# Performance work log

Measured on AMD Instinct MI355X. Metric: run time of the kernel, lower is better.

Reference implementation:

```python
import jax, jax.numpy as jnp
import numpy as np

B, T, C = 2, 2048, 2048
H = 16
ROPE_DIM, NOPE_DIM, V_DIM = 64, 64, 128
HEAD_DIM = NOPE_DIM + ROPE_DIM  # 128
Q_RANK, KV_RANK = 1536, 512


def setup_inputs() -> dict:
    key = jax.random.key(0)
    ks = jax.random.split(key, 8)
    std = 0.02
    return {
        "x": jax.random.normal(ks[0], (B, T, C), jnp.float32),
        "cos": jax.random.normal(ks[1], (1, T, 1, ROPE_DIM // 2), jnp.float32),
        "sin": jax.random.normal(ks[2], (1, T, 1, ROPE_DIM // 2), jnp.float32),
        "wq_down": jax.random.normal(ks[3], (Q_RANK, C), jnp.float32) * std,
        "wq_up": jax.random.normal(ks[4], (H * HEAD_DIM, Q_RANK), jnp.float32) * std,
        "wkv_down": jax.random.normal(ks[5], (KV_RANK, C), jnp.float32) * std,
        "wkv_up": jax.random.normal(ks[6], (H * (HEAD_DIM + V_DIM), KV_RANK), jnp.float32) * std,
        "wo": jax.random.normal(ks[7], (C, H * V_DIM), jnp.float32) * std,
    }


def _rope(x, cos, sin):
    # x: [B, T, H, rope_dim]
    d = x.shape[-1] // 2
    x1, x2 = x[..., :d], x[..., d:]
    return jnp.concatenate([x1 * cos + x2 * sin, -x1 * sin + x2 * cos], axis=-1)


def _rms_norm(x):
    eps = jnp.finfo(x.dtype).eps
    return x * jax.lax.rsqrt(jnp.mean(jnp.square(x), axis=-1, keepdims=True) + eps)


def reference(x, cos, sin, wq_down, wq_up, wkv_down, wkv_up, wo):
    # Low-rank q projection
    q = jnp.einsum('btc,rc,dr->btd', x, wq_down, wq_up)
    q = q.reshape(B, T, H, HEAD_DIM)
    q_nope, q_rope = q[..., :NOPE_DIM], q[..., NOPE_DIM:]
    # Low-rank kv projection (naive decompression)
    kv = jnp.einsum('btc,rc,dr->btd', x, wkv_down, wkv_up)
    kv = kv.reshape(B, T, H, HEAD_DIM + V_DIM)
    k_nope = kv[..., :NOPE_DIM]
    k_rope = kv[..., NOPE_DIM:HEAD_DIM]
    v = kv[..., HEAD_DIM:]
    # Partial RoPE on the rope sub-dims only
    q_rope = _rope(q_rope, cos, sin)
    k_rope = _rope(k_rope, cos, sin)
    q = _rms_norm(jnp.concatenate([q_nope, q_rope], axis=-1))
    k = _rms_norm(jnp.concatenate([k_nope, k_rope], axis=-1))
    # Causal SDPA: [B, H, T, T]
    scale = 1.0 / jnp.sqrt(jnp.float32(HEAD_DIM))
    scores = jnp.einsum('bthd,bshd->bhts', q, k) * scale
    causal = jnp.tril(jnp.ones((T, T), dtype=bool))
    scores = jnp.where(causal, scores, jnp.finfo(scores.dtype).min)
    probs = jax.nn.softmax(scores, axis=-1)
    y = jnp.einsum('bhts,bshd->bthd', probs, v).reshape(B, T, H * V_DIM)
    return y @ wo.T
```

## Files before the change

kernel.cpp:

```cpp
#include <hip/hip_runtime.h>
#include <hip/hip_bf16.h>
#include <math.h>
#include <type_traits>

#define AS1 __attribute__((address_space(1)))
#define AS3 __attribute__((address_space(3)))

typedef __bf16  bf16x8 __attribute__((ext_vector_type(8)));
typedef float   f32x4  __attribute__((ext_vector_type(4)));
typedef __hip_bfloat16 bf16;

#define MFMA16x16x32 __builtin_amdgcn_mfma_f32_16x16x32_bf16

__device__ __forceinline__ void gload16(const void* g, void* l) {
  __builtin_amdgcn_global_load_lds((const AS1 void*)g, (AS3 void*)l, 16, 0, 0);
}

__device__ __forceinline__ unsigned short bfbits(float v) {
  return __builtin_bit_cast(unsigned short, __float2bfloat16(v));
}

struct CastArgs {
  const float4* src[6];
  ushort4* dst[6];
  unsigned bound[6];
};

__global__ __launch_bounds__(256) void f2bf_multi(CastArgs a) {
  unsigned i = blockIdx.x * 256 + threadIdx.x;
  if (i >= a.bound[5]) return;
  unsigned lo = 0;
  int s = 0;
#pragma unroll
  for (int k = 0; k < 5; k++) {
    if (i >= a.bound[k]) { s = k + 1; lo = a.bound[k]; }
  }
  unsigned idx = i - lo;
  float4 v = a.src[s][idx];
  ushort4 o;
  o.x = bfbits(v.x); o.y = bfbits(v.y); o.z = bfbits(v.z); o.w = bfbits(v.w);
  a.dst[s][idx] = o;
}

template <typename OutT>
__global__ __launch_bounds__(256, 3) void gemm_bt(const bf16* __restrict__ A,
                                                  const bf16* __restrict__ W,
                                                  OutT* __restrict__ Cp,
                                                  int M, int N, int K, int lda) {
  __shared__ __align__(16) bf16 As[128 * 32];
  __shared__ __align__(16) bf16 Ws[128 * 32];
  const int t = threadIdx.x;
  const int w = t >> 6, lane = t & 63;
  const int quad = lane >> 4, l16 = lane & 15;
  const int wr = (w >> 1) * 64, wc = (w & 1) * 64;
  const size_t m0 = (size_t)blockIdx.x * 128;
  const size_t n0 = (size_t)blockIdx.y * 128;
  const int rowS = t >> 2;
  const int kch  = (t & 3) * 8;

  f32x4 acc[4][4];
#pragma unroll
  for (int i = 0; i < 4; i++)
#pragma unroll
    for (int j = 0; j < 4; j++) acc[i][j] = f32x4{0.f, 0.f, 0.f, 0.f};

  for (int k0 = 0; k0 < K; k0 += 32) {
    __syncthreads();
    gload16(A + (m0 + rowS) * (size_t)lda + k0 + kch,      (char*)As + w * 1024);
    gload16(A + (m0 + rowS + 64) * (size_t)lda + k0 + kch, (char*)As + 4096 + w * 1024);
    gload16(W + (n0 + rowS) * (size_t)K + k0 + kch,        (char*)Ws + w * 1024);
    gload16(W + (n0 + rowS + 64) * (size_t)K + k0 + kch,   (char*)Ws + 4096 + w * 1024);
    __syncthreads();

    bf16x8 af[4], bw[4];
#pragma unroll
    for (int i = 0; i < 4; i++)
      af[i] = *(const bf16x8*)(As + (wr + i * 16 + l16) * 32 + quad * 8);
#pragma unroll
    for (int j = 0; j < 4; j++)
      bw[j] = *(const bf16x8*)(Ws + (wc + j * 16 + l16) * 32 + quad * 8);
#pragma unroll
    for (int i = 0; i < 4; i++)
#pragma unroll
      for (int j = 0; j < 4; j++)
        acc[i][j] = MFMA16x16x32(af[i], bw[j], acc[i][j], 0, 0, 0);
  }

#pragma unroll
  for (int i = 0; i < 4; i++)
#pragma unroll
    for (int j = 0; j < 4; j++)
#pragma unroll
      for (int r = 0; r < 4; r++) {
        size_t row = m0 + wr + i * 16 + quad * 4 + r;
        size_t col = n0 + wc + j * 16 + l16;
        float v = acc[i][j][r];
        if constexpr (std::is_same<OutT, float>::value)
          Cp[row * N + col] = v;
        else
          Cp[row * N + col] = __float2bfloat16(v);
      }
}

__global__ __launch_bounds__(256, 3) void gemm_kvup(const bf16* __restrict__ A,
                                                    const bf16* __restrict__ W,
                                                    bf16* __restrict__ kvraw,
                                                    bf16* __restrict__ vT) {
  __shared__ __align__(16) bf16 As[128 * 32];
  __shared__ __align__(16) bf16 Ws[128 * 32];
  const int t = threadIdx.x;
  const int w = t >> 6, lane = t & 63;
  const int quad = lane >> 4, l16 = lane & 15;
  const int wr = (w >> 1) * 64, wc = (w & 1) * 64;
  const size_t m0 = (size_t)blockIdx.x * 128;
  const int n0 = (int)blockIdx.y * 128;
  const int rowS = t >> 2;
  const int kch  = (t & 3) * 8;
  const int K = 512, lda = 2048;

  f32x4 acc[4][4];
#pragma unroll
  for (int i = 0; i < 4; i++)
#pragma unroll
    for (int j = 0; j < 4; j++) acc[i][j] = f32x4{0.f, 0.f, 0.f, 0.f};

  for (int k0 = 0; k0 < K; k0 += 32) {
    __syncthreads();
    gload16(A + (m0 + rowS) * (size_t)lda + k0 + kch,        (char*)As + w * 1024);
    gload16(A + (m0 + rowS + 64) * (size_t)lda + k0 + kch,   (char*)As + 4096 + w * 1024);
    gload16(W + ((size_t)n0 + rowS) * K + k0 + kch,          (char*)Ws + w * 1024);
    gload16(W + ((size_t)n0 + rowS + 64) * K + k0 + kch,     (char*)Ws + 4096 + w * 1024);
    __syncthreads();

    bf16x8 af[4], bw[4];
#pragma unroll
    for (int i = 0; i < 4; i++)
      af[i] = *(const bf16x8*)(As + (wr + i * 16 + l16) * 32 + quad * 8);
#pragma unroll
    for (int j = 0; j < 4; j++)
      bw[j] = *(const bf16x8*)(Ws + (wc + j * 16 + l16) * 32 + quad * 8);
#pragma unroll
    for (int i = 0; i < 4; i++)
#pragma unroll
      for (int j = 0; j < 4; j++)
        acc[i][j] = MFMA16x16x32(af[i], bw[j], acc[i][j], 0, 0, 0);
  }

  if ((n0 & 128) == 0) {
#pragma unroll
    for (int i = 0; i < 4; i++)
#pragma unroll
      for (int j = 0; j < 4; j++)
#pragma unroll
        for (int r = 0; r < 4; r++) {
          size_t row = m0 + wr + i * 16 + quad * 4 + r;
          size_t col = (size_t)n0 + wc + j * 16 + l16;
          kvraw[row * 4096 + col] = __float2bfloat16(acc[i][j][r]);
        }
  } else {
    const int h = n0 >> 8;
#pragma unroll
    for (int i = 0; i < 4; i++) {
      size_t row = m0 + wr + i * 16 + quad * 4;
      int bb = (int)(row >> 11), tloc = (int)(row & 2047);
#pragma unroll
      for (int j = 0; j < 4; j++) {
        int d = wc + j * 16 + l16;
        ushort4 v4;
        v4.x = bfbits(acc[i][j][0]);
        v4.y = bfbits(acc[i][j][1]);
        v4.z = bfbits(acc[i][j][2]);
        v4.w = bfbits(acc[i][j][3]);
        *(ushort4*)(vT + ((size_t)(bb * 16 + h) * 128 + d) * 2048 + tloc) = v4;
      }
    }
  }
}

__global__ __launch_bounds__(256) void rope_rms(const bf16* __restrict__ qraw,
                                                const bf16* __restrict__ kvraw,
                                                const float* __restrict__ cosp,
                                                const float* __restrict__ sinp,
                                                bf16* __restrict__ qn,
                                                bf16* __restrict__ kn) {
  const int bt = blockIdx.x;
  const int w = threadIdx.x >> 6, lane = threadIdx.x & 63;
  const int h = blockIdx.y * 4 + w;
  const int tt = bt & 2047;
  const float c = cosp[tt * 32 + (lane & 31)];
  const float s = sinp[tt * 32 + (lane & 31)];
  const float inv128 = 1.0f / 128.0f;
  const float eps = 1.1920929e-7f;

  {
    const bf16* base = qraw + (size_t)bt * 2048 + h * 128;
    float a = (float)base[lane];
    float o = (float)base[64 + lane];
    float partner = __shfl_xor(o, 32);
    float orope = (lane < 32) ? (o * c + partner * s) : (o * c - partner * s);
    float ss = a * a + orope * orope;
#pragma unroll
    for (int off = 1; off < 64; off <<= 1) ss += __shfl_xor(ss, off);
    float rn = rsqrtf(ss * inv128 + eps);
    bf16* outp = qn + ((size_t)bt * 16 + h) * 128;
    outp[lane] = __float2bfloat16(a * rn);
    outp[64 + lane] = __float2bfloat16(orope * rn);
  }
  {
    const bf16* base = kvraw + (size_t)bt * 4096 + h * 256;
    float a = (float)base[lane];
    float o = (float)base[64 + lane];
    float partner = __shfl_xor(o, 32);
    float orope = (lane < 32) ? (o * c + partner * s) : (o * c - partner * s);
    float ss = a * a + orope * orope;
#pragma unroll
    for (int off = 1; off < 64; off <<= 1) ss += __shfl_xor(ss, off);
    float rn = rsqrtf(ss * inv128 + eps);
    bf16* outp = kn + ((size_t)bt * 16 + h) * 128;
    outp[lane] = __float2bfloat16(a * rn);
    outp[64 + lane] = __float2bfloat16(orope * rn);
  }
}

__global__ __launch_bounds__(256, 2) void attn_kernel(const bf16* __restrict__ qn,
                                                      const bf16* __restrict__ kn,
                                                      const bf16* __restrict__ vT,
                                                      bf16* __restrict__ y) {
  __shared__ __align__(16) bf16 Ks[2 * 64 * 128];
  __shared__ __align__(16) bf16 Vs[2 * 128 * 64];
  __shared__ __align__(16) bf16 Ps[4 * 16 * 64];
  const int t = threadIdx.x, w = t >> 6, lane = t & 63;
  const int quad = lane >> 4, l16 = lane & 15;
  const int b = blockIdx.x >> 4, h = blockIdx.x & 15;
  const int pr = (int)blockIdx.y;
  const int T_ = 2048, H_ = 16;
  const float K1 = 0.08838834764831845f * 1.4426950408889634f;
  const float K2 = -12.0f * 1.4426950408889634f;

  const int cgk = l16 ^ ((w * 4 + quad) & 7);
  const char* kg0 = (const char*)(kn + ((size_t)(b * T_) * H_ + h) * 128)
                    + (size_t)(w * 4 + quad) * 4096 + (size_t)cgk * 16;
  const int vrow = w * 8 + (lane >> 3);
  const int cgv = (lane & 7) ^ (vrow & 7);
  const char* vg0 = (const char*)(vT + ((size_t)(b * H_ + h) * 128 + vrow) * T_)
                    + (size_t)cgv * 16;

  auto stage = [&](auto bufc, int it2) {
    constexpr int BUF = decltype(bufc)::value;
    const size_t koff = (size_t)it2 * 262144;
    const size_t voff = (size_t)it2 * 128;
#pragma unroll
    for (int is = 0; is < 4; ++is)
      gload16(kg0 + koff + (size_t)is * 65536,
              (char*)Ks + BUF * 16384 + is * 4096 + w * 1024);
#pragma unroll
    for (int is = 0; is < 4; ++is)
      gload16(vg0 + voff + (size_t)is * 131072,
              (char*)Vs + BUF * 16384 + is * 4096 + w * 1024);
  };

  auto body = [&](auto bufc, int it, int nt, int xb,
                  bf16x8* qf, f32x4* yacc, float* lrow) {
    constexpr int BUF = decltype(bufc)::value;
    if (it + 1 < nt) {
      stage(std::integral_constant<int, 1 - BUF>{}, it + 1);
      __asm__ volatile("s_waitcnt vmcnt(8)" ::: "memory");
    } else {
      __asm__ volatile("s_waitcnt vmcnt(0)" ::: "memory");
    }
    __asm__ volatile("s_barrier" ::: "memory");

    f32x4 sacc[4];
#pragma unroll
    for (int cg = 0; cg < 4; cg++) sacc[cg] = f32x4{0.f, 0.f, 0.f, 0.f};
    __builtin_amdgcn_s_setprio(1);
#pragma unroll
    for (int cg = 0; cg < 4; ++cg) {
#pragma unroll
      for (int ks = 0; ks < 4; ++ks) {
        const int pos = (ks * 4 + quad) ^ (l16 & 7);
        const bf16x8 kf = *(const bf16x8*)((const char*)Ks + BUF * 16384 +
                                           (cg * 16 + l16) * 256 + pos * 16);
        sacc[cg] = MFMA16x16x32(qf[ks], kf, sacc[cg], 0, 0, 0);
      }
    }
    __builtin_amdgcn_s_setprio(0);

    const bool diag = (it == xb);
    float p[4][4];
#pragma unroll
    for (int cg = 0; cg < 4; ++cg)
#pragma unroll
      for (int r = 0; r < 4; ++r) {
        float e;
        if (diag && (cg * 16 + l16 > w * 16 + quad * 4 + r))
          e = 0.0f;
        else
          e = exp2f(fmaf(sacc[cg][r], K1, K2));
        p[cg][r] = e;
        lrow[r] += e;
      }

#pragma unroll
    for (int cg = 0; cg < 4; cg++)
#pragma unroll
      for (int r = 0; r < 4; r++) {
        const int row = quad * 4 + r;
        const int col = cg * 16 + l16;
        Ps[w * 1024 + row * 64 + (((col >> 3) ^ (row & 7)) << 3) + (col & 7)] =
            __float2bfloat16(p[cg][r]);
      }
    __asm__ volatile("s_waitcnt lgkmcnt(0)" ::: "memory");

    bf16x8 pf[2];
#pragma unroll
    for (int k2 = 0; k2 < 2; k2++)
      pf[k2] = *(const bf16x8*)(&Ps[w * 1024 + l16 * 64 +
                                    (((k2 * 4 + quad) ^ (l16 & 7)) << 3)]);
    __builtin_amdgcn_s_setprio(1);
#pragma unroll
    for (int dg = 0; dg < 8; dg++) {
#pragma unroll
      for (int k2 = 0; k2 < 2; k2++) {
        const int pos = (k2 * 4 + quad) ^ (l16 & 7);
        const bf16x8 vf = *(const bf16x8*)((const char*)Vs + BUF * 16384 +
                                           (dg * 16 + l16) * 128 + pos * 16);
        yacc[dg] = MFMA16x16x32(pf[k2], vf, yacc[dg], 0, 0, 0);
      }
    }
    __builtin_amdgcn_s_setprio(0);
    __asm__ volatile("s_barrier" ::: "memory");
  };

  const std::integral_constant<int, 0> c0{};
  const std::integral_constant<int, 1> c1{};

  for (int sidx = 0; sidx < 2; ++sidx) {
    const int xb = sidx ? pr : (31 - pr);
    const int q0 = xb * 64;
    const int nt = xb + 1;

    bf16x8 qf[4];
    {
      const bf16* qbase = qn + ((size_t)(b * T_ + q0 + w * 16 + l16) * H_ + h) * 128;
#pragma unroll
      for (int ks = 0; ks < 4; ks++) qf[ks] = *(const bf16x8*)(qbase + ks * 32 + quad * 8);
    }
    f32x4 yacc[8];
#pragma unroll
    for (int i = 0; i < 8; i++) yacc[i] = f32x4{0.f, 0.f, 0.f, 0.f};
    float lrow[4] = {0.f, 0.f, 0.f, 0.f};

    stage(c0, 0);
    int it = 0;
    for (; it + 2 <= nt; it += 2) {
      body(c0, it, nt, xb, qf, yacc, lrow);
      body(c1, it + 1, nt, xb, qf, yacc, lrow);
    }
    if (it < nt) body(c0, it, nt, xb, qf, yacc, lrow);

#pragma unroll
    for (int off = 1; off < 16; off <<= 1)
#pragma unroll
      for (int r = 0; r < 4; r++) lrow[r] += __shfl_xor(lrow[r], off);
#pragma unroll
    for (int r = 0; r < 4; r++) {
      float inv = 1.0f / lrow[r];
      size_t qrow = (size_t)(b * T_ + q0 + w * 16 + quad * 4 + r);
      bf16* outp = y + qrow * 2048 + h * 128;
#pragma unroll
      for (int dg = 0; dg < 8; dg++)
        outp[dg * 16 + l16] = __float2bfloat16(yacc[dg][r] * inv);
    }
  }
}

extern "C" void kernel_launch(void* const* d_in, const int* in_sizes, int n_in,
                              void* d_out, int out_size, void* d_ws, size_t ws_size,
                              hipStream_t stream) {
  (void)in_sizes; (void)n_in; (void)out_size; (void)ws_size;
  const float* x    = (const float*)d_in[0];
  const float* cosp = (const float*)d_in[1];
  const float* sinp = (const float*)d_in[2];
  const float* wqd  = (const float*)d_in[3];
  const float* wqu  = (const float*)d_in[4];
  const float* wkvd = (const float*)d_in[5];
  const float* wkvu = (const float*)d_in[6];
  const float* wo   = (const float*)d_in[7];
  float* out = (float*)d_out;

  char* ws = (char*)d_ws;
  size_t off = 0;
  auto alloc = [&](size_t elems) { bf16* p = (bf16*)(ws + off); off += elems * 2; return p; };
  bf16* xb      = alloc((size_t)4096 * 2048);
  bf16* wqdB    = alloc((size_t)1536 * 2048);
  bf16* wkvdB   = alloc((size_t)512 * 2048);
  bf16* wquB    = alloc((size_t)2048 * 1536);
  bf16* wkvuB   = alloc((size_t)4096 * 512);
  bf16* woB     = alloc((size_t)2048 * 2048);
  bf16* qkvdown = alloc((size_t)4096 * 2048);
  bf16* qraw    = alloc((size_t)4096 * 2048);
  bf16* kvraw   = alloc((size_t)4096 * 4096);
  bf16* qnb     = alloc((size_t)4096 * 16 * 128);
  bf16* knb     = alloc((size_t)4096 * 16 * 128);
  bf16* vTb     = alloc((size_t)2 * 16 * 128 * 2048);
  bf16* yb      = alloc((size_t)4096 * 2048);

  CastArgs ca;
  const float* srcs[6] = {x, wqd, wkvd, wqu, wkvu, wo};
  bf16* dsts[6]        = {xb, wqdB, wkvdB, wquB, wkvuB, woB};
  size_t cnts[6] = {(size_t)4096 * 2048, (size_t)1536 * 2048, (size_t)512 * 2048,
                    (size_t)2048 * 1536, (size_t)4096 * 512,  (size_t)2048 * 2048};
  unsigned cum = 0;
  for (int i = 0; i < 6; i++) {
    ca.src[i] = (const float4*)srcs[i];
    ca.dst[i] = (ushort4*)dsts[i];
    cum += (unsigned)(cnts[i] / 4);
    ca.bound[i] = cum;
  }
  f2bf_multi<<<dim3((cum + 255) / 256), 256, 0, stream>>>(ca);

  gemm_bt<bf16><<<dim3(32, 16), 256, 0, stream>>>(xb, wqdB, qkvdown, 4096, 2048, 2048, 2048);
  gemm_bt<bf16><<<dim3(32, 16), 256, 0, stream>>>(qkvdown, wquB, qraw, 4096, 2048, 1536, 2048);
  gemm_kvup<<<dim3(32, 32), 256, 0, stream>>>(qkvdown + 1536, wkvuB, kvraw, vTb);
  rope_rms<<<dim3(4096, 4), 256, 0, stream>>>(qraw, kvraw, cosp, sinp, qnb, knb);
  attn_kernel<<<dim3(32, 16), 256, 0, stream>>>(qnb, knb, vTb, yb);
  gemm_bt<float><<<dim3(32, 16), 256, 0, stream>>>(yb, woB, out, 4096, 2048, 2048, 2048);
}
```

Before: 375.2 us.

## Single-buffer attention LDS via register staging, one query tile per block

The attention kernel switches from double-buffered direct global-to-LDS loads to register-staged prefetch with a single LDS buffer. That halves K/V shared memory, and launch bounds rise from 2 to 4 blocks per SM. Each block now handles one query tile instead of a paired long/short tile, using a permuted causal ordering over a doubled grid. The aim is higher occupancy and more parallelism, at the cost of extra registers, two barriers per iteration and less load/compute overlap.

```diff
diff --git a/kernel.cpp b/kernel.cpp
--- a/kernel.cpp
+++ b/kernel.cpp
@@ -222,17 +222,25 @@
   }
 }
 
-__global__ __launch_bounds__(256, 2) void attn_kernel(const bf16* __restrict__ qn,
+__global__ __launch_bounds__(256, 4) void attn_kernel(const bf16* __restrict__ qn,
                                                       const bf16* __restrict__ kn,
                                                       const bf16* __restrict__ vT,
                                                       bf16* __restrict__ y) {
-  __shared__ __align__(16) bf16 Ks[2 * 64 * 128];
-  __shared__ __align__(16) bf16 Vs[2 * 128 * 64];
+  __shared__ __align__(16) bf16 Ks[64 * 128];
+  __shared__ __align__(16) bf16 Vs[128 * 64];
   __shared__ __align__(16) bf16 Ps[4 * 16 * 64];
   const int t = threadIdx.x, w = t >> 6, lane = t & 63;
   const int quad = lane >> 4, l16 = lane & 15;
   const int b = blockIdx.x >> 4, h = blockIdx.x & 15;
-  const int pr = (int)blockIdx.y;
+  const int yy = (int)blockIdx.y;
+  const int y0 = yy & 7, k4 = yy >> 3;
+  int xb;
+  if (k4 == 0) xb = 31 - y0;
+  else if (k4 == 1) xb = y0;
+  else if (k4 == 2) xb = 23 - y0;
+  else xb = 8 + y0;
+  const int q0 = xb * 64;
+  const int nt = xb + 1;
   const int T_ = 2048, H_ = 16;
   const float K1 = 0.08838834764831845f * 1.4426950408889634f;
   const float K2 = -12.0f * 1.4426950408889634f;
@@ -244,31 +252,43 @@
   const int cgv = (lane & 7) ^ (vrow & 7);
   const char* vg0 = (const char*)(vT + ((size_t)(b * H_ + h) * 128 + vrow) * T_)
                     + (size_t)cgv * 16;
-
-  auto stage = [&](auto bufc, int it2) {
-    constexpr int BUF = decltype(bufc)::value;
-    const size_t koff = (size_t)it2 * 262144;
-    const size_t voff = (size_t)it2 * 128;
+  char* kl0 = (char*)Ks + w * 1024 + lane * 16;
+  char* vl0 = (char*)Vs + w * 1024 + lane * 16;
+
+  bf16x8 kst[4], vst[4];
+  auto issue_loads = [&](int it2) {
 #pragma unroll
     for (int is = 0; is < 4; ++is)
-      gload16(kg0 + koff + (size_t)is * 65536,
-              (char*)Ks + BUF * 16384 + is * 4096 + w * 1024);
+      kst[is] = *(const bf16x8*)(kg0 + (size_t)it2 * 262144 + (size_t)is * 65536);
 #pragma unroll
     for (int is = 0; is < 4; ++is)
-      gload16(vg0 + voff + (size_t)is * 131072,
-              (char*)Vs + BUF * 16384 + is * 4096 + w * 1024);
+      vst[is] = *(const bf16x8*)(vg0 + (size_t)it2 * 128 + (size_t)is * 131072);
   };
-
-  auto body = [&](auto bufc, int it, int nt, int xb,
-                  bf16x8* qf, f32x4* yacc, float* lrow) {
-    constexpr int BUF = decltype(bufc)::value;
-    if (it + 1 < nt) {
-      stage(std::integral_constant<int, 1 - BUF>{}, it + 1);
-      __asm__ volatile("s_waitcnt vmcnt(8)" ::: "memory");
-    } else {
-      __asm__ volatile("s_waitcnt vmcnt(0)" ::: "memory");
-    }
-    __asm__ volatile("s_barrier" ::: "memory");
+  auto write_lds = [&]() {
+#pragma unroll
+    for (int is = 0; is < 4; ++is) *(bf16x8*)(kl0 + is * 4096) = kst[is];
+#pragma unroll
+    for (int is = 0; is < 4; ++is) *(bf16x8*)(vl0 + is * 4096) = vst[is];
+  };
+
+  bf16x8 qf[4];
+  {
+    const bf16* qbase = qn + ((size_t)(b * T_ + q0 + w * 16 + l16) * H_ + h) * 128;
+#pragma unroll
+    for (int ks = 0; ks < 4; ks++) qf[ks] = *(const bf16x8*)(qbase + ks * 32 + quad * 8);
+  }
+  f32x4 yacc[8];
+#pragma unroll
+  for (int i = 0; i < 8; i++) yacc[i] = f32x4{0.f, 0.f, 0.f, 0.f};
+  float lrow[4] = {0.f, 0.f, 0.f, 0.f};
+
+  issue_loads(0);
+  write_lds();
+  __asm__ volatile("s_barrier" ::: "memory");
+
+  for (int it = 0; it < nt; ++it) {
+    const bool more = (it + 1 < nt);
+    if (more) issue_loads(it + 1);
 
     f32x4 sacc[4];
 #pragma unroll
@@ -279,7 +299,7 @@
 #pragma unroll
       for (int ks = 0; ks < 4; ++ks) {
         const int pos = (ks * 4 + quad) ^ (l16 & 7);
-        const bf16x8 kf = *(const bf16x8*)((const char*)Ks + BUF * 16384 +
+        const bf16x8 kf = *(const bf16x8*)((const char*)Ks +
                                            (cg * 16 + l16) * 256 + pos * 16);
         sacc[cg] = MFMA16x16x32(qf[ks], kf, sacc[cg], 0, 0, 0);
       }
@@ -323,55 +343,32 @@
 #pragma unroll
       for (int k2 = 0; k2 < 2; k2++) {
         const int pos = (k2 * 4 + quad) ^ (l16 & 7);
-        const bf16x8 vf = *(const bf16x8*)((const char*)Vs + BUF * 16384 +
+        const bf16x8 vf = *(const bf16x8*)((const char*)Vs +
                                            (dg * 16 + l16) * 128 + pos * 16);
         yacc[dg] = MFMA16x16x32(pf[k2], vf, yacc[dg], 0, 0, 0);
       }
     }
     __builtin_amdgcn_s_setprio(0);
-    __asm__ volatile("s_barrier" ::: "memory");
-  };
-
-  const std::integral_constant<int, 0> c0{};
-  const std::integral_constant<int, 1> c1{};
-
-  for (int sidx = 0; sidx < 2; ++sidx) {
-    const int xb = sidx ? pr : (31 - pr);
-    const int q0 = xb * 64;
-    const int nt = xb + 1;
-
-    bf16x8 qf[4];
-    {
-      const bf16* qbase = qn + ((size_t)(b * T_ + q0 + w * 16 + l16) * H_ + h) * 128;
-#pragma unroll
-      for (int ks = 0; ks < 4; ks++) qf[ks] = *(const bf16x8*)(qbase + ks * 32 + quad * 8);
+
+    if (more) {
+      __asm__ volatile("s_barrier" ::: "memory");
+      write_lds();
+      __asm__ volatile("s_barrier" ::: "memory");
     }
-    f32x4 yacc[8];
-#pragma unroll
-    for (int i = 0; i < 8; i++) yacc[i] = f32x4{0.f, 0.f, 0.f, 0.f};
-    float lrow[4] = {0.f, 0.f, 0.f, 0.f};
-
-    stage(c0, 0);
-    int it = 0;
-    for (; it + 2 <= nt; it += 2) {
-      body(c0, it, nt, xb, qf, yacc, lrow);
-      body(c1, it + 1, nt, xb, qf, yacc, lrow);
-    }
-    if (it < nt) body(c0, it, nt, xb, qf, yacc, lrow);
-
-#pragma unroll
-    for (int off = 1; off < 16; off <<= 1)
-#pragma unroll
-      for (int r = 0; r < 4; r++) lrow[r] += __shfl_xor(lrow[r], off);
-#pragma unroll
-    for (int r = 0; r < 4; r++) {
-      float inv = 1.0f / lrow[r];
-      size_t qrow = (size_t)(b * T_ + q0 + w * 16 + quad * 4 + r);
-      bf16* outp = y + qrow * 2048 + h * 128;
-#pragma unroll
-      for (int dg = 0; dg < 8; dg++)
-        outp[dg * 16 + l16] = __float2bfloat16(yacc[dg][r] * inv);
-    }
+  }
+
+#pragma unroll
+  for (int off = 1; off < 16; off <<= 1)
+#pragma unroll
+    for (int r = 0; r < 4; r++) lrow[r] += __shfl_xor(lrow[r], off);
+#pragma unroll
+  for (int r = 0; r < 4; r++) {
+    float inv = 1.0f / lrow[r];
+    size_t qrow = (size_t)(b * T_ + q0 + w * 16 + quad * 4 + r);
+    bf16* outp = y + qrow * 2048 + h * 128;
+#pragma unroll
+    for (int dg = 0; dg < 8; dg++)
+      outp[dg * 16 + l16] = __float2bfloat16(yacc[dg][r] * inv);
   }
 }
 
@@ -424,6 +421,6 @@
   gemm_bt<bf16><<<dim3(32, 16), 256, 0, stream>>>(qkvdown, wquB, qraw, 4096, 2048, 1536, 2048);
   gemm_kvup<<<dim3(32, 32), 256, 0, stream>>>(qkvdown + 1536, wkvuB, kvraw, vTb);
   rope_rms<<<dim3(4096, 4), 256, 0, stream>>>(qraw, kvraw, cosp, sinp, qnb, knb);
-  attn_kernel<<<dim3(32, 16), 256, 0, stream>>>(qnb, knb, vTb, yb);
+  attn_kernel<<<dim3(32, 32), 256, 0, stream>>>(qnb, knb, vTb, yb);
   gemm_bt<float><<<dim3(32, 16), 256, 0, stream>>>(yb, woB, out, 4096, 2048, 2048, 2048);
 }
```

Measured after the change: 447.6 us. 19.3% more time.

## Replace GEMMs with 256-row tiles and a 4-stage async LDS pipeline

Applied to the files above, without the earlier changes.

Replaces the 128x128 single-buffered GEMM kernels with a templated 512-thread kernel using 256x128 or 256x256 tiles. It keeps four K-stages in flight through direct global-to-LDS loads and counted vmcnt waits, so loads overlap MFMA work, and raises wave priority around the MFMAs. The kv-up projection is folded into the same template, with one tile covering a whole head's k and v columns. The cost is larger LDS and register use per block, and the grid shrinks to 256 blocks, which may leave some CUs idle.

```diff
diff --git a/kernel.cpp b/kernel.cpp
--- a/kernel.cpp
+++ b/kernel.cpp
@@ -19,6 +19,9 @@
 __device__ __forceinline__ unsigned short bfbits(float v) {
   return __builtin_bit_cast(unsigned short, __float2bfloat16(v));
 }
+
+#define LGKM0 __asm__ volatile("s_waitcnt lgkmcnt(0)" ::: "memory")
+#define BARRIER __builtin_amdgcn_s_barrier()
 
 struct CastArgs {
   const float4* src[6];
@@ -42,136 +45,160 @@
   a.dst[s][idx] = o;
 }
 
-template <typename OutT>
-__global__ __launch_bounds__(256, 3) void gemm_bt(const bf16* __restrict__ A,
+template <int BM, int BN, typename OutT, bool KVUP>
+__global__ __launch_bounds__(512, 2) void gemm256(const bf16* __restrict__ A,
                                                   const bf16* __restrict__ W,
                                                   OutT* __restrict__ Cp,
-                                                  int M, int N, int K, int lda) {
-  __shared__ __align__(16) bf16 As[128 * 32];
-  __shared__ __align__(16) bf16 Ws[128 * 32];
-  const int t = threadIdx.x;
-  const int w = t >> 6, lane = t & 63;
+                                                  bf16* __restrict__ vT,
+                                                  int N, int K, int lda) {
+  constexpr int WGN = (BN == 256) ? 4 : 2;
+  constexpr int WGM = 8 / WGN;
+  constexpr int MF = BM / WGM / 16;
+  constexpr int NF = BN / WGN / 16;
+  constexpr int LA = BM / 128;
+  constexpr int LB = BN / 128;
+  constexpr int L  = LA + LB;
+  constexpr int ASUB = BM * 64;
+  constexpr int BSUB = BN * 64;
+  __shared__ __align__(16) char lds[4 * (ASUB + BSUB)];
+  char* ldsA = lds;
+  char* ldsB = lds + 4 * ASUB;
+
+  const int t = threadIdx.x, w = t >> 6, lane = t & 63;
   const int quad = lane >> 4, l16 = lane & 15;
-  const int wr = (w >> 1) * 64, wc = (w & 1) * 64;
-  const size_t m0 = (size_t)blockIdx.x * 128;
-  const size_t n0 = (size_t)blockIdx.y * 128;
-  const int rowS = t >> 2;
-  const int kch  = (t & 3) * 8;
-
-  f32x4 acc[4][4];
-#pragma unroll
-  for (int i = 0; i < 4; i++)
-#pragma unroll
-    for (int j = 0; j < 4; j++) acc[i][j] = f32x4{0.f, 0.f, 0.f, 0.f};
-
-  for (int k0 = 0; k0 < K; k0 += 32) {
-    __syncthreads();
-    gload16(A + (m0 + rowS) * (size_t)lda + k0 + kch,      (char*)As + w * 1024);
-    gload16(A + (m0 + rowS + 64) * (size_t)lda + k0 + kch, (char*)As + 4096 + w * 1024);
-    gload16(W + (n0 + rowS) * (size_t)K + k0 + kch,        (char*)Ws + w * 1024);
-    gload16(W + (n0 + rowS + 64) * (size_t)K + k0 + kch,   (char*)Ws + 4096 + w * 1024);
-    __syncthreads();
-
-    bf16x8 af[4], bw[4];
-#pragma unroll
-    for (int i = 0; i < 4; i++)
-      af[i] = *(const bf16x8*)(As + (wr + i * 16 + l16) * 32 + quad * 8);
-#pragma unroll
-    for (int j = 0; j < 4; j++)
-      bw[j] = *(const bf16x8*)(Ws + (wc + j * 16 + l16) * 32 + quad * 8);
-#pragma unroll
-    for (int i = 0; i < 4; i++)
-#pragma unroll
-      for (int j = 0; j < 4; j++)
-        acc[i][j] = MFMA16x16x32(af[i], bw[j], acc[i][j], 0, 0, 0);
-  }
-
-#pragma unroll
-  for (int i = 0; i < 4; i++)
-#pragma unroll
-    for (int j = 0; j < 4; j++)
-#pragma unroll
-      for (int r = 0; r < 4; r++) {
-        size_t row = m0 + wr + i * 16 + quad * 4 + r;
-        size_t col = n0 + wc + j * 16 + l16;
-        float v = acc[i][j][r];
-        if constexpr (std::is_same<OutT, float>::value)
-          Cp[row * N + col] = v;
-        else
-          Cp[row * N + col] = __float2bfloat16(v);
-      }
-}
-
-__global__ __launch_bounds__(256, 3) void gemm_kvup(const bf16* __restrict__ A,
-                                                    const bf16* __restrict__ W,
-                                                    bf16* __restrict__ kvraw,
-                                                    bf16* __restrict__ vT) {
-  __shared__ __align__(16) bf16 As[128 * 32];
-  __shared__ __align__(16) bf16 Ws[128 * 32];
-  const int t = threadIdx.x;
-  const int w = t >> 6, lane = t & 63;
-  const int quad = lane >> 4, l16 = lane & 15;
-  const int wr = (w >> 1) * 64, wc = (w & 1) * 64;
-  const size_t m0 = (size_t)blockIdx.x * 128;
-  const int n0 = (int)blockIdx.y * 128;
-  const int rowS = t >> 2;
-  const int kch  = (t & 3) * 8;
-  const int K = 512, lda = 2048;
-
-  f32x4 acc[4][4];
-#pragma unroll
-  for (int i = 0; i < 4; i++)
-#pragma unroll
-    for (int j = 0; j < 4; j++) acc[i][j] = f32x4{0.f, 0.f, 0.f, 0.f};
-
-  for (int k0 = 0; k0 < K; k0 += 32) {
-    __syncthreads();
-    gload16(A + (m0 + rowS) * (size_t)lda + k0 + kch,        (char*)As + w * 1024);
-    gload16(A + (m0 + rowS + 64) * (size_t)lda + k0 + kch,   (char*)As + 4096 + w * 1024);
-    gload16(W + ((size_t)n0 + rowS) * K + k0 + kch,          (char*)Ws + w * 1024);
-    gload16(W + ((size_t)n0 + rowS + 64) * K + k0 + kch,     (char*)Ws + 4096 + w * 1024);
-    __syncthreads();
-
-    bf16x8 af[4], bw[4];
-#pragma unroll
-    for (int i = 0; i < 4; i++)
-      af[i] = *(const bf16x8*)(As + (wr + i * 16 + l16) * 32 + quad * 8);
-#pragma unroll
-    for (int j = 0; j < 4; j++)
-      bw[j] = *(const bf16x8*)(Ws + (wc + j * 16 + l16) * 32 + quad * 8);
-#pragma unroll
-    for (int i = 0; i < 4; i++)
-#pragma unroll
-      for (int j = 0; j < 4; j++)
-        acc[i][j] = MFMA16x16x32(af[i], bw[j], acc[i][j], 0, 0, 0);
-  }
-
-  if ((n0 & 128) == 0) {
-#pragma unroll
-    for (int i = 0; i < 4; i++)
-#pragma unroll
-      for (int j = 0; j < 4; j++)
-#pragma unroll
-        for (int r = 0; r < 4; r++) {
-          size_t row = m0 + wr + i * 16 + quad * 4 + r;
-          size_t col = (size_t)n0 + wc + j * 16 + l16;
-          kvraw[row * 4096 + col] = __float2bfloat16(acc[i][j][r]);
+  const int wm = w / WGN, wn = w % WGN;
+  const int wrow = wm * (BM / WGM), wcol = wn * (BN / WGN);
+  const size_t m0 = (size_t)blockIdx.x * BM;
+  const size_t n0 = (size_t)blockIdx.y * BN;
+  const int NT = K / 32;
+
+  const bf16* asrc[LA];
+#pragma unroll
+  for (int st = 0; st < LA; ++st) {
+    int slot = st * 512 + w * 64 + lane;
+    int row = slot % BM, chunk = slot / BM;
+    asrc[st] = A + (m0 + row) * (size_t)lda + chunk * 8;
+  }
+  const bf16* bsrc[LB];
+#pragma unroll
+  for (int st = 0; st < LB; ++st) {
+    int slot = st * 512 + w * 64 + lane;
+    int row = slot % BN, chunk = slot / BN;
+    bsrc[st] = W + (n0 + row) * (size_t)K + chunk * 8;
+  }
+
+  auto stage = [&](int s, int c) {
+#pragma unroll
+    for (int st = 0; st < LA; ++st)
+      gload16(asrc[st] + s * 32, ldsA + c * ASUB + st * 8192 + w * 1024);
+#pragma unroll
+    for (int st = 0; st < LB; ++st)
+      gload16(bsrc[st] + s * 32, ldsB + c * BSUB + st * 8192 + w * 1024);
+  };
+
+  f32x4 acc[MF][NF];
+#pragma unroll
+  for (int i = 0; i < MF; i++)
+#pragma unroll
+    for (int j = 0; j < NF; j++) acc[i][j] = f32x4{0.f, 0.f, 0.f, 0.f};
+
+  auto compute = [&](int c) {
+    bf16x8 af[MF], bw[NF];
+#pragma unroll
+    for (int nf = 0; nf < NF; ++nf)
+      bw[nf] = *(const bf16x8*)(ldsB + c * BSUB +
+                                (quad * BN + wcol + nf * 16 + l16) * 16);
+#pragma unroll
+    for (int mf = 0; mf < MF; ++mf)
+      af[mf] = *(const bf16x8*)(ldsA + c * ASUB +
+                                (quad * BM + wrow + mf * 16 + l16) * 16);
+    __builtin_amdgcn_s_setprio(1);
+#pragma unroll
+    for (int mf = 0; mf < MF; ++mf)
+#pragma unroll
+      for (int nf = 0; nf < NF; ++nf)
+        acc[mf][nf] = MFMA16x16x32(af[mf], bw[nf], acc[mf][nf], 0, 0, 0);
+    __builtin_amdgcn_s_setprio(0);
+  };
+
+#define VM_STEADY do { if constexpr (L == 4) \
+    __asm__ volatile("s_waitcnt vmcnt(12)" ::: "memory"); \
+  else __asm__ volatile("s_waitcnt vmcnt(9)" ::: "memory"); } while (0)
+#define VM_2 do { if constexpr (L == 4) \
+    __asm__ volatile("s_waitcnt vmcnt(8)" ::: "memory"); \
+  else __asm__ volatile("s_waitcnt vmcnt(6)" ::: "memory"); } while (0)
+#define VM_1 do { if constexpr (L == 4) \
+    __asm__ volatile("s_waitcnt vmcnt(4)" ::: "memory"); \
+  else __asm__ volatile("s_waitcnt vmcnt(3)" ::: "memory"); } while (0)
+#define VM_0 __asm__ volatile("s_waitcnt vmcnt(0)" ::: "memory")
+
+  stage(0, 0); stage(1, 1); stage(2, 2);
+
+  for (int s4 = 0; s4 < NT - 4; s4 += 4) {
+#pragma unroll
+    for (int jj = 0; jj < 4; ++jj) {
+      stage(s4 + jj + 3, (jj + 3) & 3);
+      VM_STEADY;
+      BARRIER;
+      compute(jj);
+      LGKM0;
+      BARRIER;
+    }
+  }
+  stage(NT - 1, 3);
+  VM_STEADY; BARRIER; compute(0); LGKM0; BARRIER;
+  VM_2;      BARRIER; compute(1); LGKM0; BARRIER;
+  VM_1;      BARRIER; compute(2); LGKM0; BARRIER;
+  VM_0;      BARRIER; compute(3);
+
+#undef VM_STEADY
+#undef VM_2
+#undef VM_1
+#undef VM_0
+
+  if constexpr (!KVUP) {
+#pragma unroll
+    for (int mf = 0; mf < MF; ++mf)
+#pragma unroll
+      for (int nf = 0; nf < NF; ++nf)
+#pragma unroll
+        for (int r = 0; r < 4; ++r) {
+          size_t row = m0 + wrow + mf * 16 + quad * 4 + r;
+          size_t col = n0 + wcol + nf * 16 + l16;
+          float v = acc[mf][nf][r];
+          if constexpr (std::is_same<OutT, float>::value)
+            Cp[row * N + col] = v;
+          else
+            Cp[row * N + col] = __float2bfloat16(v);
         }
   } else {
-    const int h = n0 >> 8;
-#pragma unroll
-    for (int i = 0; i < 4; i++) {
-      size_t row = m0 + wr + i * 16 + quad * 4;
-      int bb = (int)(row >> 11), tloc = (int)(row & 2047);
-#pragma unroll
-      for (int j = 0; j < 4; j++) {
-        int d = wc + j * 16 + l16;
-        ushort4 v4;
-        v4.x = bfbits(acc[i][j][0]);
-        v4.y = bfbits(acc[i][j][1]);
-        v4.z = bfbits(acc[i][j][2]);
-        v4.w = bfbits(acc[i][j][3]);
-        *(ushort4*)(vT + ((size_t)(bb * 16 + h) * 128 + d) * 2048 + tloc) = v4;
+    const int head = (int)(n0 >> 8);
+    if (wcol < 128) {
+#pragma unroll
+      for (int mf = 0; mf < MF; ++mf)
+#pragma unroll
+        for (int nf = 0; nf < NF; ++nf)
+#pragma unroll
+          for (int r = 0; r < 4; ++r) {
+            size_t row = m0 + wrow + mf * 16 + quad * 4 + r;
+            size_t col = n0 + wcol + nf * 16 + l16;
+            Cp[row * 4096 + col] = __float2bfloat16(acc[mf][nf][r]);
+          }
+    } else {
+#pragma unroll
+      for (int mf = 0; mf < MF; ++mf) {
+        size_t row = m0 + wrow + mf * 16 + quad * 4;
+        int bb = (int)(row >> 11), tloc = (int)(row & 2047);
+#pragma unroll
+        for (int nf = 0; nf < NF; ++nf) {
+          int d = wcol - 128 + nf * 16 + l16;
+          ushort4 v4;
+          v4.x = bfbits(acc[mf][nf][0]);
+          v4.y = bfbits(acc[mf][nf][1]);
+          v4.z = bfbits(acc[mf][nf][2]);
+          v4.w = bfbits(acc[mf][nf][3]);
+          *(ushort4*)(vT + ((size_t)(bb * 16 + head) * 128 + d) * 2048 + tloc) = v4;
+        }
       }
     }
   }
@@ -420,10 +447,14 @@
   }
   f2bf_multi<<<dim3((cum + 255) / 256), 256, 0, stream>>>(ca);
 
-  gemm_bt<bf16><<<dim3(32, 16), 256, 0, stream>>>(xb, wqdB, qkvdown, 4096, 2048, 2048, 2048);
-  gemm_bt<bf16><<<dim3(32, 16), 256, 0, stream>>>(qkvdown, wquB, qraw, 4096, 2048, 1536, 2048);
-  gemm_kvup<<<dim3(32, 32), 256, 0, stream>>>(qkvdown + 1536, wkvuB, kvraw, vTb);
+  gemm256<256, 128, bf16, false><<<dim3(16, 16), 512, 0, stream>>>(
+      xb, wqdB, qkvdown, nullptr, 2048, 2048, 2048);
+  gemm256<256, 128, bf16, false><<<dim3(16, 16), 512, 0, stream>>>(
+      qkvdown, wquB, qraw, nullptr, 2048, 1536, 2048);
+  gemm256<256, 256, bf16, true><<<dim3(16, 16), 512, 0, stream>>>(
+      qkvdown + 1536, wkvuB, kvraw, vTb, 4096, 512, 2048);
   rope_rms<<<dim3(4096, 4), 256, 0, stream>>>(qraw, kvraw, cosp, sinp, qnb, knb);
   attn_kernel<<<dim3(32, 16), 256, 0, stream>>>(qnb, knb, vTb, yb);
-  gemm_bt<float><<<dim3(32, 16), 256, 0, stream>>>(yb, woB, out, 4096, 2048, 2048, 2048);
-}
+  gemm256<256, 128, float, false><<<dim3(16, 16), 512, 0, stream>>>(
+      yb, woB, out, nullptr, 2048, 2048, 2048);
+}
```

After: 451.2 us. 1.2x slower.

## Double GEMM K-tile to 64 with XOR-swizzled LDS and XCD-aware block remap

Applied to the files above, without the earlier changes.

Rewrites the GEMM kernels to load 64-wide K slices per iteration, which halves the number of barrier pairs, and stores tiles in LDS with an XOR swizzle to avoid bank conflicts on fragment reads. A 1D grid is remapped so that consecutive blocks are spread across XCDs for better L2 locality, and MFMA sections are wrapped in s_setprio. The cost is twice the LDS per block (32KB), which may reduce occupancy, and a hardcoded 32-row-tile mapping that assumes M=4096.

```diff
diff --git a/kernel.cpp b/kernel.cpp
--- a/kernel.cpp
+++ b/kernel.cpp
@@ -43,20 +43,31 @@
 }
 
 template <typename OutT>
-__global__ __launch_bounds__(256, 3) void gemm_bt(const bf16* __restrict__ A,
-                                                  const bf16* __restrict__ W,
-                                                  OutT* __restrict__ Cp,
-                                                  int M, int N, int K, int lda) {
-  __shared__ __align__(16) bf16 As[128 * 32];
-  __shared__ __align__(16) bf16 Ws[128 * 32];
+__global__ __launch_bounds__(256, 3) void gemm_bt64(const bf16* __restrict__ A,
+                                                    const bf16* __restrict__ W,
+                                                    OutT* __restrict__ Cp,
+                                                    int N, int K, int lda) {
+  __shared__ __align__(16) bf16 As[128 * 64];
+  __shared__ __align__(16) bf16 Ws[128 * 64];
   const int t = threadIdx.x;
   const int w = t >> 6, lane = t & 63;
   const int quad = lane >> 4, l16 = lane & 15;
   const int wr = (w >> 1) * 64, wc = (w & 1) * 64;
-  const size_t m0 = (size_t)blockIdx.x * 128;
-  const size_t n0 = (size_t)blockIdx.y * 128;
-  const int rowS = t >> 2;
-  const int kch  = (t & 3) * 8;
+  const unsigned bid = blockIdx.x, nwg = gridDim.x;
+  const unsigned swz = (bid & 7) * (nwg >> 3) + (bid >> 3);
+  const size_t m0 = (size_t)(swz & 31) * 128;
+  const size_t n0 = (size_t)(swz >> 5) * 128;
+
+  const int r8 = lane >> 3;
+  const int cg = (lane & 7) ^ r8;
+  const bf16* aSrc = A + (m0 + w * 8 + r8) * (size_t)lda + cg * 8;
+  const bf16* wSrc = W + (n0 + w * 8 + r8) * (size_t)K + cg * 8;
+  const size_t sA = (size_t)32 * lda, sW = (size_t)32 * K;
+
+  const int cx0 = ((quad) ^ (l16 & 7)) << 4;
+  const int cx1 = ((4 + quad) ^ (l16 & 7)) << 4;
+  const char* aRb = (const char*)As + (wr + l16) * 128;
+  const char* bRb = (const char*)Ws + (wc + l16) * 128;
 
   f32x4 acc[4][4];
 #pragma unroll
@@ -64,26 +75,37 @@
 #pragma unroll
     for (int j = 0; j < 4; j++) acc[i][j] = f32x4{0.f, 0.f, 0.f, 0.f};
 
-  for (int k0 = 0; k0 < K; k0 += 32) {
+  for (int k0 = 0; k0 < K; k0 += 64) {
     __syncthreads();
-    gload16(A + (m0 + rowS) * (size_t)lda + k0 + kch,      (char*)As + w * 1024);
-    gload16(A + (m0 + rowS + 64) * (size_t)lda + k0 + kch, (char*)As + 4096 + w * 1024);
-    gload16(W + (n0 + rowS) * (size_t)K + k0 + kch,        (char*)Ws + w * 1024);
-    gload16(W + (n0 + rowS + 64) * (size_t)K + k0 + kch,   (char*)Ws + 4096 + w * 1024);
+#pragma unroll
+    for (int is = 0; is < 4; ++is)
+      gload16(aSrc + is * sA, (char*)As + is * 4096 + w * 1024);
+#pragma unroll
+    for (int is = 0; is < 4; ++is)
+      gload16(wSrc + is * sW, (char*)Ws + is * 4096 + w * 1024);
+    aSrc += 64; wSrc += 64;
     __syncthreads();
 
-    bf16x8 af[4], bw[4];
+    bf16x8 af[4][2], bw[4][2];
+#pragma unroll
+    for (int i = 0; i < 4; i++) {
+      af[i][0] = *(const bf16x8*)(aRb + i * 2048 + cx0);
+      af[i][1] = *(const bf16x8*)(aRb + i * 2048 + cx1);
+    }
+#pragma unroll
+    for (int j = 0; j < 4; j++) {
+      bw[j][0] = *(const bf16x8*)(bRb + j * 2048 + cx0);
+      bw[j][1] = *(const bf16x8*)(bRb + j * 2048 + cx1);
+    }
+    __builtin_amdgcn_s_setprio(1);
 #pragma unroll
     for (int i = 0; i < 4; i++)
-      af[i] = *(const bf16x8*)(As + (wr + i * 16 + l16) * 32 + quad * 8);
-#pragma unroll
-    for (int j = 0; j < 4; j++)
-      bw[j] = *(const bf16x8*)(Ws + (wc + j * 16 + l16) * 32 + quad * 8);
-#pragma unroll
-    for (int i = 0; i < 4; i++)
 #pragma unroll
       for (int j = 0; j < 4; j++)
-        acc[i][j] = MFMA16x16x32(af[i], bw[j], acc[i][j], 0, 0, 0);
+#pragma unroll
+        for (int ks = 0; ks < 2; ks++)
+          acc[i][j] = MFMA16x16x32(af[i][ks], bw[j][ks], acc[i][j], 0, 0, 0);
+    __builtin_amdgcn_s_setprio(0);
   }
 
 #pragma unroll
@@ -102,21 +124,32 @@
       }
 }
 
-__global__ __launch_bounds__(256, 3) void gemm_kvup(const bf16* __restrict__ A,
-                                                    const bf16* __restrict__ W,
-                                                    bf16* __restrict__ kvraw,
-                                                    bf16* __restrict__ vT) {
-  __shared__ __align__(16) bf16 As[128 * 32];
-  __shared__ __align__(16) bf16 Ws[128 * 32];
+__global__ __launch_bounds__(256, 3) void gemm_kvup64(const bf16* __restrict__ A,
+                                                      const bf16* __restrict__ W,
+                                                      bf16* __restrict__ kvraw,
+                                                      bf16* __restrict__ vT) {
+  __shared__ __align__(16) bf16 As[128 * 64];
+  __shared__ __align__(16) bf16 Ws[128 * 64];
   const int t = threadIdx.x;
   const int w = t >> 6, lane = t & 63;
   const int quad = lane >> 4, l16 = lane & 15;
   const int wr = (w >> 1) * 64, wc = (w & 1) * 64;
-  const size_t m0 = (size_t)blockIdx.x * 128;
-  const int n0 = (int)blockIdx.y * 128;
-  const int rowS = t >> 2;
-  const int kch  = (t & 3) * 8;
   const int K = 512, lda = 2048;
+  const unsigned bid = blockIdx.x, nwg = gridDim.x;
+  const unsigned swz = (bid & 7) * (nwg >> 3) + (bid >> 3);
+  const size_t m0 = (size_t)(swz & 31) * 128;
+  const int n0 = (int)(swz >> 5) * 128;
+
+  const int r8 = lane >> 3;
+  const int cg = (lane & 7) ^ r8;
+  const bf16* aSrc = A + (m0 + w * 8 + r8) * (size_t)lda + cg * 8;
+  const bf16* wSrc = W + ((size_t)n0 + w * 8 + r8) * (size_t)K + cg * 8;
+  const size_t sA = (size_t)32 * lda, sW = (size_t)32 * K;
+
+  const int cx0 = ((quad) ^ (l16 & 7)) << 4;
+  const int cx1 = ((4 + quad) ^ (l16 & 7)) << 4;
+  const char* aRb = (const char*)As + (wr + l16) * 128;
+  const char* bRb = (const char*)Ws + (wc + l16) * 128;
 
   f32x4 acc[4][4];
 #pragma unroll
@@ -124,26 +157,37 @@
 #pragma unroll
     for (int j = 0; j < 4; j++) acc[i][j] = f32x4{0.f, 0.f, 0.f, 0.f};
 
-  for (int k0 = 0; k0 < K; k0 += 32) {
+  for (int k0 = 0; k0 < K; k0 += 64) {
     __syncthreads();
-    gload16(A + (m0 + rowS) * (size_t)lda + k0 + kch,        (char*)As + w * 1024);
-    gload16(A + (m0 + rowS + 64) * (size_t)lda + k0 + kch,   (char*)As + 4096 + w * 1024);
-    gload16(W + ((size_t)n0 + rowS) * K + k0 + kch,          (char*)Ws + w * 1024);
-    gload16(W + ((size_t)n0 + rowS + 64) * K + k0 + kch,     (char*)Ws + 4096 + w * 1024);
+#pragma unroll
+    for (int is = 0; is < 4; ++is)
+      gload16(aSrc + is * sA, (char*)As + is * 4096 + w * 1024);
+#pragma unroll
+    for (int is = 0; is < 4; ++is)
+      gload16(wSrc + is * sW, (char*)Ws + is * 4096 + w * 1024);
+    aSrc += 64; wSrc += 64;
     __syncthreads();
 
-    bf16x8 af[4], bw[4];
+    bf16x8 af[4][2], bw[4][2];
+#pragma unroll
+    for (int i = 0; i < 4; i++) {
+      af[i][0] = *(const bf16x8*)(aRb + i * 2048 + cx0);
+      af[i][1] = *(const bf16x8*)(aRb + i * 2048 + cx1);
+    }
+#pragma unroll
+    for (int j = 0; j < 4; j++) {
+      bw[j][0] = *(const bf16x8*)(bRb + j * 2048 + cx0);
+      bw[j][1] = *(const bf16x8*)(bRb + j * 2048 + cx1);
+    }
+    __builtin_amdgcn_s_setprio(1);
 #pragma unroll
     for (int i = 0; i < 4; i++)
-      af[i] = *(const bf16x8*)(As + (wr + i * 16 + l16) * 32 + quad * 8);
-#pragma unroll
-    for (int j = 0; j < 4; j++)
-      bw[j] = *(const bf16x8*)(Ws + (wc + j * 16 + l16) * 32 + quad * 8);
-#pragma unroll
-    for (int i = 0; i < 4; i++)
 #pragma unroll
       for (int j = 0; j < 4; j++)
-        acc[i][j] = MFMA16x16x32(af[i], bw[j], acc[i][j], 0, 0, 0);
+#pragma unroll
+        for (int ks = 0; ks < 2; ks++)
+          acc[i][j] = MFMA16x16x32(af[i][ks], bw[j][ks], acc[i][j], 0, 0, 0);
+    __builtin_amdgcn_s_setprio(0);
   }
 
   if ((n0 & 128) == 0) {
@@ -420,10 +464,10 @@
   }
   f2bf_multi<<<dim3((cum + 255) / 256), 256, 0, stream>>>(ca);
 
-  gemm_bt<bf16><<<dim3(32, 16), 256, 0, stream>>>(xb, wqdB, qkvdown, 4096, 2048, 2048, 2048);
-  gemm_bt<bf16><<<dim3(32, 16), 256, 0, stream>>>(qkvdown, wquB, qraw, 4096, 2048, 1536, 2048);
-  gemm_kvup<<<dim3(32, 32), 256, 0, stream>>>(qkvdown + 1536, wkvuB, kvraw, vTb);
+  gemm_bt64<bf16><<<dim3(512), 256, 0, stream>>>(xb, wqdB, qkvdown, 2048, 2048, 2048);
+  gemm_bt64<bf16><<<dim3(512), 256, 0, stream>>>(qkvdown, wquB, qraw, 2048, 1536, 2048);
+  gemm_kvup64<<<dim3(1024), 256, 0, stream>>>(qkvdown + 1536, wkvuB, kvraw, vTb);
   rope_rms<<<dim3(4096, 4), 256, 0, stream>>>(qraw, kvraw, cosp, sinp, qnb, knb);
   attn_kernel<<<dim3(32, 16), 256, 0, stream>>>(qnb, knb, vTb, yb);
-  gemm_bt<float><<<dim3(32, 16), 256, 0, stream>>>(yb, woB, out, 4096, 2048, 2048, 2048);
-}
+  gemm_bt64<float><<<dim3(512), 256, 0, stream>>>(yb, woB, out, 2048, 2048, 2048);
+}
```

New measurement: 369.3 us. No clear change (-1.6%).
